# Optimization experiments

Hardware: AMD Instinct MI355X
Metric: run time of the kernel (lower is better)

The kernel has to match this reference:

```python
import jax, jax.numpy as jnp
import numpy as np
from jax import lax

STRIDE = (1, 1)
PAD = ((1, 1), (1, 1))


def ste_sign(x, alpha):
    # Forward value is sign(x); backward flows through tanh(alpha*x) (STE).
    q = jnp.sign(x)
    e = jnp.tanh(alpha * x)
    return lax.stop_gradient(q - e) + e


def dwconv(x, w, channels):
    # x: [N,C,H,W], w: [C,1,k,j] (OIHW), depthwise => feature_group_count=C
    return lax.conv_general_dilated(
        x, w, window_strides=STRIDE, padding=PAD,
        dimension_numbers=("NCHW", "OIHW", "NCHW"),
        feature_group_count=channels)


def setup_inputs() -> dict:
    key = jax.random.key(0)
    k1, k2 = jax.random.split(key)
    x = jax.random.normal(k1, (32, 128, 112, 112), dtype=jnp.float32)
    weight = jax.random.normal(k2, (128, 1, 3, 3), dtype=jnp.float32)
    alpha_x = jnp.ones((), dtype=jnp.float32)
    alpha_w = jnp.ones((), dtype=jnp.float32)
    return {"x": x, "weight": weight, "alpha_x": alpha_x, "alpha_w": alpha_w}


def reference(x, weight, alpha_x, alpha_w):
    channels = weight.shape[0]
    xq = ste_sign(x, alpha_x)          # quantized activations (sign, STE)
    wq = ste_sign(weight, alpha_w)     # quantized weights (sign, STE)
    # out = dwconv(sign(x), w) + dwconv(x, sign(w)); matches the two einsums
    out = dwconv(xq, weight, channels) + dwconv(x, wq, channels)
    return out
```

## Files before the change

### kernel.cpp

```cpp
#include <hip/hip_runtime.h>


#define CH   128
#define HH   112
#define WW   112
#define NW4  28
#define PLANE (HH * WW)

__device__ __forceinline__ float fsign(float v) {
    return (v > 0.0f) ? 1.0f : ((v < 0.0f) ? -1.0f : 0.0f);
}

__device__ __forceinline__ float sign_mul(float v, float w) {
    unsigned int vb = __float_as_uint(v);
    float r = __uint_as_float(__float_as_uint(w) ^ (vb & 0x80000000u));
    return ((vb << 1) == 0u) ? 0.0f : r;
}

__global__ __launch_bounds__(256) void bisign_dwconv_kernel(
    const float* __restrict__ x,
    const float* __restrict__ wt,
    float* __restrict__ out)
{
    const int plane = blockIdx.x;
    const int c = plane & (CH - 1);

    const float* __restrict__ xc = x   + (size_t)plane * PLANE;
    float* __restrict__       oc = out + (size_t)plane * PLANE;

    float Wv[9], SWv[9];
#pragma unroll
    for (int k = 0; k < 9; ++k) {
        const float wv = wt[c * 9 + k];
        Wv[k]  = wv;
        SWv[k] = fsign(wv);
    }

    for (int idx = threadIdx.x; idx < HH * NW4; idx += 256) {
        const int h   = idx / NW4;
        const int w4  = idx - h * NW4;
        const int col = w4 * 4;

        float acc0 = 0.f, acc1 = 0.f, acc2 = 0.f, acc3 = 0.f;

#pragma unroll
        for (int dr = 0; dr < 3; ++dr) {
            const int r = h + dr - 1;
            float v0, v1, v2, v3, v4, v5;
            if (r >= 0 && r < HH) {
                const float* row = xc + r * WW + col;
                const float4 m = *reinterpret_cast<const float4*>(row);
                v1 = m.x; v2 = m.y; v3 = m.z; v4 = m.w;
                v0 = (w4 > 0)       ? row[-1] : 0.0f;
                v5 = (w4 < NW4 - 1) ? row[4]  : 0.0f;
            } else {
                v0 = v1 = v2 = v3 = v4 = v5 = 0.0f;
            }

            const float w0 = Wv[dr * 3 + 0], w1 = Wv[dr * 3 + 1], w2 = Wv[dr * 3 + 2];
            const float q0 = SWv[dr * 3 + 0], q1 = SWv[dr * 3 + 1], q2 = SWv[dr * 3 + 2];

            acc0 += sign_mul(v0, w0) + v0 * q0;
            acc0 += sign_mul(v1, w1) + v1 * q1;
            acc0 += sign_mul(v2, w2) + v2 * q2;

            acc1 += sign_mul(v1, w0) + v1 * q0;
            acc1 += sign_mul(v2, w1) + v2 * q1;
            acc1 += sign_mul(v3, w2) + v3 * q2;

            acc2 += sign_mul(v2, w0) + v2 * q0;
            acc2 += sign_mul(v3, w1) + v3 * q1;
            acc2 += sign_mul(v4, w2) + v4 * q2;

            acc3 += sign_mul(v3, w0) + v3 * q0;
            acc3 += sign_mul(v4, w1) + v4 * q1;
            acc3 += sign_mul(v5, w2) + v5 * q2;
        }

        float4 o;
        o.x = acc0; o.y = acc1; o.z = acc2; o.w = acc3;
        *reinterpret_cast<float4*>(oc + h * WW + col) = o;
    }
}

extern "C" void kernel_launch(void* const* d_in, const int* in_sizes, int n_in,
                              void* d_out, int out_size, void* d_ws, size_t ws_size,
                              hipStream_t stream) {
    const float* x  = (const float*)d_in[0];
    const float* wt = (const float*)d_in[1];
    float* out = (float*)d_out;

    const int N = in_sizes[0] / (CH * PLANE);
    const int nblocks = N * CH;

    bisign_dwconv_kernel<<<nblocks, 256, 0, stream>>>(x, wt, out);
}
```

Before: 400.5 us.

## Compute seven output rows per thread with rolling register row window

Each thread now computes a vertical strip of seven output rows for one 4-column group and keeps a rolling three-row register window, so each input row is loaded and sign-converted once rather than three times. The block size becomes 448 threads (28 columns by 16 row groups), which exactly covers the plane, so the strided loop and the index division go away. The sign-times-weight term is rewritten as a precomputed sign of the input multiplied by the weight, and both terms are fused into FMAs. Register pressure rises and the block shape changes occupancy. The kernel was likely memory-bound already, so the reduced reload traffic may mostly come out of L1/L2 rather than HBM.

New measurement: 358.4 us. 1.12x faster.

```diff
diff --git a/kernel.cpp b/kernel.cpp
--- a/kernel.cpp
+++ b/kernel.cpp
@@ -1,23 +1,65 @@
 #include <hip/hip_runtime.h>
 
 
-#define CH   128
-#define HH   112
-#define WW   112
-#define NW4  28
+#define CH    128
+#define HH    112
+#define WW    112
+#define NW4   28
 #define PLANE (HH * WW)
+#define RPT   7
+#define NRG   (HH / RPT)
+#define NTHR  (NW4 * NRG)
 
-__device__ __forceinline__ float fsign(float v) {
-    return (v > 0.0f) ? 1.0f : ((v < 0.0f) ? -1.0f : 0.0f);
+__device__ __forceinline__ float sgn(float v) {
+    float one = __uint_as_float(0x3f800000u | (__float_as_uint(v) & 0x80000000u));
+    return (v == 0.0f) ? 0.0f : one;
 }
 
-__device__ __forceinline__ float sign_mul(float v, float w) {
-    unsigned int vb = __float_as_uint(v);
-    float r = __uint_as_float(__float_as_uint(w) ^ (vb & 0x80000000u));
-    return ((vb << 1) == 0u) ? 0.0f : r;
-}
+#define LOADROW(r, V)                                                 \
+  {                                                                   \
+    const int rr_ = (r);                                              \
+    if (rr_ >= 0 && rr_ < HH) {                                       \
+      const float* row_ = xc + rr_ * WW + col;                        \
+      const float4 m_ = *reinterpret_cast<const float4*>(row_);       \
+      V[1] = m_.x; V[2] = m_.y; V[3] = m_.z; V[4] = m_.w;             \
+      V[0] = has_l ? row_[-1] : 0.0f;                                 \
+      V[5] = has_r ? row_[4]  : 0.0f;                                 \
+    } else {                                                          \
+      V[0] = V[1] = V[2] = V[3] = V[4] = V[5] = 0.0f;                 \
+    }                                                                 \
+  }
 
-__global__ __launch_bounds__(256) void bisign_dwconv_kernel(
+#define SIGNROW(V, S)                                                 \
+  { S[0]=sgn(V[0]); S[1]=sgn(V[1]); S[2]=sgn(V[2]);                   \
+    S[3]=sgn(V[3]); S[4]=sgn(V[4]); S[5]=sgn(V[5]); }
+
+#define ACCR(V, S, dr)                                                        \
+    a0 = fmaf(S[0], W[3*(dr)+0], fmaf(V[0], Q[3*(dr)+0], a0));                \
+    a0 = fmaf(S[1], W[3*(dr)+1], fmaf(V[1], Q[3*(dr)+1], a0));                \
+    a0 = fmaf(S[2], W[3*(dr)+2], fmaf(V[2], Q[3*(dr)+2], a0));                \
+    a1 = fmaf(S[1], W[3*(dr)+0], fmaf(V[1], Q[3*(dr)+0], a1));                \
+    a1 = fmaf(S[2], W[3*(dr)+1], fmaf(V[2], Q[3*(dr)+1], a1));                \
+    a1 = fmaf(S[3], W[3*(dr)+2], fmaf(V[3], Q[3*(dr)+2], a1));                \
+    a2 = fmaf(S[2], W[3*(dr)+0], fmaf(V[2], Q[3*(dr)+0], a2));                \
+    a2 = fmaf(S[3], W[3*(dr)+1], fmaf(V[3], Q[3*(dr)+1], a2));                \
+    a2 = fmaf(S[4], W[3*(dr)+2], fmaf(V[4], Q[3*(dr)+2], a2));                \
+    a3 = fmaf(S[3], W[3*(dr)+0], fmaf(V[3], Q[3*(dr)+0], a3));                \
+    a3 = fmaf(S[4], W[3*(dr)+1], fmaf(V[4], Q[3*(dr)+1], a3));                \
+    a3 = fmaf(S[5], W[3*(dr)+2], fmaf(V[5], Q[3*(dr)+2], a3));
+
+#define STEP(i, VT, ST, VM, SM, VB, SB)                               \
+  {                                                                   \
+    LOADROW(rbase + (i) + 1, VB);                                     \
+    SIGNROW(VB, SB);                                                  \
+    float a0 = 0.f, a1 = 0.f, a2 = 0.f, a3 = 0.f;                     \
+    ACCR(VT, ST, 0);                                                  \
+    ACCR(VM, SM, 1);                                                  \
+    ACCR(VB, SB, 2);                                                  \
+    float4 o_; o_.x = a0; o_.y = a1; o_.z = a2; o_.w = a3;            \
+    *reinterpret_cast<float4*>(oc + (rbase + (i)) * WW + col) = o_;   \
+  }
+
+__global__ __launch_bounds__(NTHR) void bisign_dwconv_kernel(
     const float* __restrict__ x,
     const float* __restrict__ wt,
     float* __restrict__ out)
@@ -28,59 +70,35 @@
     const float* __restrict__ xc = x   + (size_t)plane * PLANE;
     float* __restrict__       oc = out + (size_t)plane * PLANE;
 
-    float Wv[9], SWv[9];
+    float W[9], Q[9];
 #pragma unroll
     for (int k = 0; k < 9; ++k) {
         const float wv = wt[c * 9 + k];
-        Wv[k]  = wv;
-        SWv[k] = fsign(wv);
+        W[k] = wv;
+        Q[k] = sgn(wv);
     }
 
-    for (int idx = threadIdx.x; idx < HH * NW4; idx += 256) {
-        const int h   = idx / NW4;
-        const int w4  = idx - h * NW4;
-        const int col = w4 * 4;
+    const int tid   = threadIdx.x;
+    const int col4  = tid % NW4;
+    const int rg    = tid / NW4;
+    const int col   = col4 * 4;
+    const int rbase = rg * RPT;
 
-        float acc0 = 0.f, acc1 = 0.f, acc2 = 0.f, acc3 = 0.f;
+    const bool has_l = (col4 > 0);
+    const bool has_r = (col4 < NW4 - 1);
 
-#pragma unroll
-        for (int dr = 0; dr < 3; ++dr) {
-            const int r = h + dr - 1;
-            float v0, v1, v2, v3, v4, v5;
-            if (r >= 0 && r < HH) {
-                const float* row = xc + r * WW + col;
-                const float4 m = *reinterpret_cast<const float4*>(row);
-                v1 = m.x; v2 = m.y; v3 = m.z; v4 = m.w;
-                v0 = (w4 > 0)       ? row[-1] : 0.0f;
-                v5 = (w4 < NW4 - 1) ? row[4]  : 0.0f;
-            } else {
-                v0 = v1 = v2 = v3 = v4 = v5 = 0.0f;
-            }
+    float V0[6], V1[6], V2[6], S0[6], S1[6], S2[6];
 
-            const float w0 = Wv[dr * 3 + 0], w1 = Wv[dr * 3 + 1], w2 = Wv[dr * 3 + 2];
-            const float q0 = SWv[dr * 3 + 0], q1 = SWv[dr * 3 + 1], q2 = SWv[dr * 3 + 2];
+    LOADROW(rbase - 1, V0); SIGNROW(V0, S0);
+    LOADROW(rbase,     V1); SIGNROW(V1, S1);
 
-            acc0 += sign_mul(v0, w0) + v0 * q0;
-            acc0 += sign_mul(v1, w1) + v1 * q1;
-            acc0 += sign_mul(v2, w2) + v2 * q2;
-
-            acc1 += sign_mul(v1, w0) + v1 * q0;
-            acc1 += sign_mul(v2, w1) + v2 * q1;
-            acc1 += sign_mul(v3, w2) + v3 * q2;
-
-            acc2 += sign_mul(v2, w0) + v2 * q0;
-            acc2 += sign_mul(v3, w1) + v3 * q1;
-            acc2 += sign_mul(v4, w2) + v4 * q2;
-
-            acc3 += sign_mul(v3, w0) + v3 * q0;
-            acc3 += sign_mul(v4, w1) + v4 * q1;
-            acc3 += sign_mul(v5, w2) + v5 * q2;
-        }
-
-        float4 o;
-        o.x = acc0; o.y = acc1; o.z = acc2; o.w = acc3;
-        *reinterpret_cast<float4*>(oc + h * WW + col) = o;
-    }
+    STEP(0, V0, S0, V1, S1, V2, S2);
+    STEP(1, V1, S1, V2, S2, V0, S0);
+    STEP(2, V2, S2, V0, S0, V1, S1);
+    STEP(3, V0, S0, V1, S1, V2, S2);
+    STEP(4, V1, S1, V2, S2, V0, S0);
+    STEP(5, V2, S2, V0, S0, V1, S1);
+    STEP(6, V0, S0, V1, S1, V2, S2);
 }
 
 extern "C" void kernel_launch(void* const* d_in, const int* in_sizes, int n_in,
@@ -93,5 +111,5 @@
     const int N = in_sizes[0] / (CH * PLANE);
     const int nblocks = N * CH;
 
-    bisign_dwconv_kernel<<<nblocks, 256, 0, stream>>>(x, wt, out);
+    bisign_dwconv_kernel<<<nblocks, NTHR, 0, stream>>>(x, wt, out);
 }
```
